# Kernel optimization log

Measured on AMD Instinct MI355X. Metric: run time of the kernel, lower is better.

## Reference

```python
import jax, jax.numpy as jnp
import numpy as np

B, T, D, H = 64, 1024, 1024, 1024  # batch, n_steps, n_in, n_hidden


def setup_inputs() -> dict:
    key = jax.random.key(0)
    k1, k2 = jax.random.split(key)
    x = jax.random.normal(k1, (B, T, D), dtype=jnp.float32)
    # BasicRNNCell kernel: [n_in + n_hidden, n_hidden], glorot-ish scale
    W = jax.random.normal(k2, (D + H, H), dtype=jnp.float32) * (1.0 / np.sqrt(D + H))
    b = jnp.zeros((H,), dtype=jnp.float32)
    return {"x": x, "W": W, "b": b}


def reference(x, W, b):
    """Vanilla RNN (tf BasicRNNCell): h_t = tanh([x_t, h_{t-1}] @ W + b).
    return_last=False -> outputs all hidden states, shape [B, T, H]."""
    Wx = W[: x.shape[-1]]   # [D, H]
    Wh = W[x.shape[-1]:]    # [H, H]
    # Precompute input projections for all steps in one big GEMM: [B, T, H]
    x_proj = jnp.einsum('btd,dh->bth', x, Wx) + b

    def step(h, xp_t):
        h_new = jnp.tanh(xp_t + h @ Wh)
        return h_new, h_new

    h0 = jnp.zeros((x.shape[0], Wh.shape[1]), dtype=x.dtype)
    # scan over time: [T, B, H]
    _, outs = jax.lax.scan(step, h0, jnp.swapaxes(x_proj, 0, 1))
    return jnp.swapaxes(outs, 0, 1)  # [B, T, H]
```

## Files before the change

kernel.cpp:

```cpp
#include <hip/hip_runtime.h>
#include <stdint.h>


#define T_LEN 1024
#define HID   1024

typedef float  f32x4  __attribute__((ext_vector_type(4)));
typedef __bf16 bf16x8 __attribute__((ext_vector_type(8)));
typedef unsigned long long u64;

__global__ __launch_bounds__(256) void xproj_gemm(
    const float* __restrict__ x, const float* __restrict__ W,
    const float* __restrict__ bias, float* __restrict__ out)
{
    __shared__ __align__(16) __bf16 As[128][40];
    __shared__ __align__(16) __bf16 Bs[128][40];

    const int bid = blockIdx.x;
    const int n0  = (bid & 7) << 7;
    const int64_t r0 = (int64_t)(bid >> 3) << 7;
    const int tid  = threadIdx.x;
    const int lane = tid & 63;
    const int w    = tid >> 6;
    const int hi   = lane >> 4, lo = lane & 15;
    const int wm   = (w >> 1) << 6, wn = (w & 1) << 6;

    f32x4 acc[4][4] = {};

    const int arow = tid >> 1, akh = (tid & 1) << 4;
    const int bk   = tid >> 3, bnh = (tid & 7) << 4;

    for (int k0 = 0; k0 < 1024; k0 += 32) {
        {
            const float* src = x + (r0 + arow) * 1024 + k0 + akh;
            bf16x8 t0, t1;
            #pragma unroll
            for (int i2 = 0; i2 < 8; ++i2) { t0[i2] = (__bf16)src[i2]; t1[i2] = (__bf16)src[8 + i2]; }
            *(bf16x8*)&As[arow][akh]     = t0;
            *(bf16x8*)&As[arow][akh + 8] = t1;
        }
        {
            const float* src = W + (int64_t)(k0 + bk) * 1024 + n0 + bnh;
            #pragma unroll
            for (int i2 = 0; i2 < 16; ++i2) {
                int col = bnh + i2;
                Bs[col][bk ^ (((col >> 4) & 3) << 3)] = (__bf16)src[i2];
            }
        }
        __syncthreads();

        bf16x8 af[4], bfr[4];
        #pragma unroll
        for (int f = 0; f < 4; ++f)
            af[f] = *(const bf16x8*)&As[wm + f * 16 + lo][hi << 3];
        #pragma unroll
        for (int f = 0; f < 4; ++f) {
            const int cswz = (((wn >> 4) + f) & 3) << 3;
            bfr[f] = *(const bf16x8*)&Bs[wn + f * 16 + lo][(hi << 3) ^ cswz];
        }
        #pragma unroll
        for (int fm = 0; fm < 4; ++fm)
            #pragma unroll
            for (int fn = 0; fn < 4; ++fn)
                acc[fm][fn] = __builtin_amdgcn_mfma_f32_16x16x32_bf16(af[fm], bfr[fn], acc[fm][fn], 0, 0, 0);
        __syncthreads();
    }

    #pragma unroll
    for (int fm = 0; fm < 4; ++fm) {
        const int64_t mrow = r0 + wm + fm * 16 + hi * 4;
        #pragma unroll
        for (int fn = 0; fn < 4; ++fn) {
            const int col = n0 + wn + fn * 16 + lo;
            const float bv = bias[col];
            #pragma unroll
            for (int r = 0; r < 4; ++r)
                out[(mrow + r) * 1024 + col] = acc[fm][fn][r] + bv;
        }
    }
}

__device__ __forceinline__ float tanh_fast(float x) {
    float e = __builtin_amdgcn_exp2f(x * 2.885390082f);
    return 1.0f - 2.0f * __builtin_amdgcn_rcpf(e + 1.0f);
}

__global__ __launch_bounds__(256) void rnn_scan(
    const float* __restrict__ W, float* __restrict__ out,
    unsigned int* __restrict__ hx)
{
    __shared__ __align__(16) __bf16 WhS[32][64][8];
    __shared__ float red[4][16][17];

    const int bid = blockIdx.x;
    const int ig  = bid >> 6;
    const int jg  = bid & 63;
    const int tid = threadIdx.x;
    const int lane = tid & 63;
    const int w   = tid >> 6;
    const int hi  = lane >> 4, lo = lane & 15;

    for (int kb = w * 8; kb < w * 8 + 8; ++kb) {
        const float* src = W + (int64_t)(1024 + kb * 32 + hi * 8) * 1024 + jg * 16 + lo;
        bf16x8 t;
        #pragma unroll
        for (int ii = 0; ii < 8; ++ii) t[ii] = (__bf16)src[(int64_t)ii * 1024];
        *(bf16x8*)&WhS[kb][lane][0] = t;
    }
    __syncthreads();

    const int64_t rstride = (int64_t)T_LEN * HID;
    const int m = tid >> 4, n = tid & 15;
    float* pobase = out + (int64_t)(ig * 16 + m) * rstride + jg * 16 + n;

    const int rd_row = ig * 16 + lo;
    const int wr_idx = (ig * 16 + m) * 1024 + jg * 16 + n;

    for (int t = 0; t < T_LEN; ++t) {
        float* po = pobase + (int64_t)t * HID;
        float xpv = *po;

        f32x4 acc = {0.f, 0.f, 0.f, 0.f};
        if (t > 0) {
            const unsigned int exptag = (unsigned int)t;
            const u64* bp = (const u64*)(hx + ((t - 1) & 1) * 65536
                                            + rd_row * 1024 + w * 256 + hi * 8);
            u64 q[32];
            bool bad;
            do {
                #pragma unroll
                for (int j = 0; j < 32; ++j)
                    q[j] = __hip_atomic_load(bp + (j >> 2) * 16 + (j & 3),
                                             __ATOMIC_RELAXED, __HIP_MEMORY_SCOPE_AGENT);
                unsigned int badm = 0;
                #pragma unroll
                for (int j = 0; j < 32; ++j) {
                    badm |= ((unsigned int)(q[j] >> 16) & 0xffffu) ^ exptag;
                    badm |= ((unsigned int)(q[j] >> 48)) ^ exptag;
                }
                bad = (badm != 0);
                if (bad) __builtin_amdgcn_s_sleep(1);
            } while (bad);

            #pragma unroll
            for (int kb2 = 0; kb2 < 8; ++kb2) {
                bf16x8 a;
                #pragma unroll
                for (int p = 0; p < 4; ++p) {
                    u64 v = q[kb2 * 4 + p];
                    a[p * 2]     = __builtin_bit_cast(__bf16, (unsigned short)(v & 0xffffu));
                    a[p * 2 + 1] = __builtin_bit_cast(__bf16, (unsigned short)((v >> 32) & 0xffffu));
                }
                acc = __builtin_amdgcn_mfma_f32_16x16x32_bf16(
                          a, *(const bf16x8*)&WhS[w * 8 + kb2][lane][0], acc, 0, 0, 0);
            }
        }

        red[w][hi * 4 + 0][lo] = acc[0];
        red[w][hi * 4 + 1][lo] = acc[1];
        red[w][hi * 4 + 2][lo] = acc[2];
        red[w][hi * 4 + 3][lo] = acc[3];
        __syncthreads();

        float s = red[0][m][n] + red[1][m][n] + red[2][m][n] + red[3][m][n];
        float h = tanh_fast(xpv + s);

        unsigned short hb = __builtin_bit_cast(unsigned short, (__bf16)h);
        __hip_atomic_store(hx + (t & 1) * 65536 + wr_idx,
                           ((unsigned int)(t + 1) << 16) | (unsigned int)hb,
                           __ATOMIC_RELAXED, __HIP_MEMORY_SCOPE_AGENT);

        *po = h;

        __syncthreads();
    }
}

extern "C" void kernel_launch(void* const* d_in, const int* in_sizes, int n_in,
                              void* d_out, int out_size, void* d_ws, size_t ws_size,
                              hipStream_t stream)
{
    const float* x    = (const float*)d_in[0];
    const float* W    = (const float*)d_in[1];
    const float* bias = (const float*)d_in[2];
    float* out = (float*)d_out;

    unsigned int* hx = (unsigned int*)d_ws;

    hipMemsetAsync(hx, 0, 524288, stream);
    xproj_gemm<<<dim3(4096), dim3(256), 0, stream>>>(x, W, bias, out);
    rnn_scan<<<dim3(256), dim3(256), 0, stream>>>(W, out, hx);
}
```

Measured before the change: 8.173 ms.

## Restructure RNN scan into 32 wide blocks with register-resident Wh and LDS-shared h

Replaces the 256-block scan, where each block handled a 16x16 output tile with a cross-wave K split, with 32 blocks of 512 threads. Each wave owns 16 output columns, keeps the full Wh column slice in registers, and runs all of K itself. Each thread loads a small slab of the previous hidden state once, and the slab is shared through swizzled LDS instead of every wave polling 32 words. The goal is fewer blocks spinning on global flags, less redundant L2 polling and no LDS reduction. The cost is far fewer CUs doing the serial per-step work and very high register pressure from holding 32 bf16x8 fragments per thread.

```diff
diff --git a/kernel.cpp b/kernel.cpp
--- a/kernel.cpp
+++ b/kernel.cpp
@@ -85,92 +85,124 @@
     return 1.0f - 2.0f * __builtin_amdgcn_rcpf(e + 1.0f);
 }
 
-__global__ __launch_bounds__(256) void rnn_scan(
+__global__ __launch_bounds__(512, 2) void rnn_scan(
     const float* __restrict__ W, float* __restrict__ out,
     unsigned int* __restrict__ hx)
 {
-    __shared__ __align__(16) __bf16 WhS[32][64][8];
-    __shared__ float red[4][16][17];
+    __shared__ __align__(16) unsigned char A_lds[16 * 2048];
 
     const int bid = blockIdx.x;
-    const int ig  = bid >> 6;
-    const int jg  = bid & 63;
+    const int ig  = bid >> 3;
+    const int jg  = bid & 7;
     const int tid = threadIdx.x;
     const int lane = tid & 63;
-    const int w   = tid >> 6;
+    const int wv  = tid >> 6;
     const int hi  = lane >> 4, lo = lane & 15;
 
-    for (int kb = w * 8; kb < w * 8 + 8; ++kb) {
-        const float* src = W + (int64_t)(1024 + kb * 32 + hi * 8) * 1024 + jg * 16 + lo;
-        bf16x8 t;
-        #pragma unroll
-        for (int ii = 0; ii < 8; ++ii) t[ii] = (__bf16)src[(int64_t)ii * 1024];
-        *(bf16x8*)&WhS[kb][lane][0] = t;
-    }
-    __syncthreads();
+    const int col = jg * 128 + wv * 16 + lo;
+    bf16x8 breg[32];
+    {
+        const float* wb = W + (int64_t)1024 * 1024 + col;
+        #pragma unroll
+        for (int kb = 0; kb < 32; ++kb) {
+            const float* src = wb + (int64_t)(kb * 32 + hi * 8) * 1024;
+            bf16x8 tf;
+            #pragma unroll
+            for (int j = 0; j < 8; ++j) tf[j] = (__bf16)src[(int64_t)j * 1024];
+            breg[kb] = tf;
+        }
+    }
+
+    const int srow = tid >> 5;
+    const int c32  = tid & 31;
+    const int slab_u64 = (ig * 16 + srow) * 512 + c32 * 16;
+    const unsigned swz_w = (unsigned)((srow & 7) << 4);
+    const unsigned kbyte0 = (unsigned)(c32 * 64);
+
+    const unsigned abase = (unsigned)(lo * 2048);
+    const unsigned axor  = (unsigned)((lo & 7) << 4);
 
     const int64_t rstride = (int64_t)T_LEN * HID;
-    const int m = tid >> 4, n = tid & 15;
-    float* pobase = out + (int64_t)(ig * 16 + m) * rstride + jg * 16 + n;
-
-    const int rd_row = ig * 16 + lo;
-    const int wr_idx = (ig * 16 + m) * 1024 + jg * 16 + n;
+    float* pr0 = out + (int64_t)(ig * 16 + hi * 4) * rstride + col;
+    const int wr0 = (ig * 16 + hi * 4) * 1024 + col;
 
     for (int t = 0; t < T_LEN; ++t) {
-        float* po = pobase + (int64_t)t * HID;
-        float xpv = *po;
-
-        f32x4 acc = {0.f, 0.f, 0.f, 0.f};
+        float xpv0 = pr0[(int64_t)t * HID];
+        float xpv1 = pr0[(int64_t)t * HID + rstride];
+        float xpv2 = pr0[(int64_t)t * HID + 2 * rstride];
+        float xpv3 = pr0[(int64_t)t * HID + 3 * rstride];
+
+        f32x4 accs = {0.f, 0.f, 0.f, 0.f};
         if (t > 0) {
             const unsigned int exptag = (unsigned int)t;
-            const u64* bp = (const u64*)(hx + ((t - 1) & 1) * 65536
-                                            + rd_row * 1024 + w * 256 + hi * 8);
-            u64 q[32];
-            bool bad;
-            do {
+            const u64* bp = (const u64*)(hx + ((t - 1) & 1) * 65536) + slab_u64;
+            u64 q[16];
+            #pragma unroll
+            for (int j = 0; j < 16; ++j)
+                q[j] = __hip_atomic_load(bp + j, __ATOMIC_RELAXED, __HIP_MEMORY_SCOPE_AGENT);
+            unsigned bad = 0;
+            #pragma unroll
+            for (int j = 0; j < 16; ++j) {
+                unsigned b = (((unsigned)(q[j] >> 16) & 0xffffu) ^ exptag)
+                           | (((unsigned)(q[j] >> 48)) ^ exptag);
+                bad |= (b ? 1u : 0u) << j;
+            }
+            while (bad) {
+                __builtin_amdgcn_s_sleep(1);
                 #pragma unroll
-                for (int j = 0; j < 32; ++j)
-                    q[j] = __hip_atomic_load(bp + (j >> 2) * 16 + (j & 3),
-                                             __ATOMIC_RELAXED, __HIP_MEMORY_SCOPE_AGENT);
-                unsigned int badm = 0;
-                #pragma unroll
-                for (int j = 0; j < 32; ++j) {
-                    badm |= ((unsigned int)(q[j] >> 16) & 0xffffu) ^ exptag;
-                    badm |= ((unsigned int)(q[j] >> 48)) ^ exptag;
-                }
-                bad = (badm != 0);
-                if (bad) __builtin_amdgcn_s_sleep(1);
-            } while (bad);
-
-            #pragma unroll
-            for (int kb2 = 0; kb2 < 8; ++kb2) {
-                bf16x8 a;
-                #pragma unroll
-                for (int p = 0; p < 4; ++p) {
-                    u64 v = q[kb2 * 4 + p];
-                    a[p * 2]     = __builtin_bit_cast(__bf16, (unsigned short)(v & 0xffffu));
-                    a[p * 2 + 1] = __builtin_bit_cast(__bf16, (unsigned short)((v >> 32) & 0xffffu));
-                }
-                acc = __builtin_amdgcn_mfma_f32_16x16x32_bf16(
-                          a, *(const bf16x8*)&WhS[w * 8 + kb2][lane][0], acc, 0, 0, 0);
-            }
-        }
-
-        red[w][hi * 4 + 0][lo] = acc[0];
-        red[w][hi * 4 + 1][lo] = acc[1];
-        red[w][hi * 4 + 2][lo] = acc[2];
-        red[w][hi * 4 + 3][lo] = acc[3];
-        __syncthreads();
-
-        float s = red[0][m][n] + red[1][m][n] + red[2][m][n] + red[3][m][n];
-        float h = tanh_fast(xpv + s);
-
-        unsigned short hb = __builtin_bit_cast(unsigned short, (__bf16)h);
-        __hip_atomic_store(hx + (t & 1) * 65536 + wr_idx,
-                           ((unsigned int)(t + 1) << 16) | (unsigned int)hb,
-                           __ATOMIC_RELAXED, __HIP_MEMORY_SCOPE_AGENT);
-
-        *po = h;
+                for (int j = 0; j < 16; ++j)
+                    if (bad & (1u << j)) {
+                        q[j] = __hip_atomic_load(bp + j, __ATOMIC_RELAXED, __HIP_MEMORY_SCOPE_AGENT);
+                        if ((((unsigned)(q[j] >> 16) & 0xffffu) == exptag) &&
+                            ((unsigned)(q[j] >> 48) == exptag))
+                            bad &= ~(1u << j);
+                    }
+            }
+            unsigned dw[16];
+            #pragma unroll
+            for (int j = 0; j < 16; ++j)
+                dw[j] = __builtin_amdgcn_perm((unsigned)(q[j] >> 32), (unsigned)q[j], 0x05040100u);
+            #pragma unroll
+            for (int i = 0; i < 4; ++i) {
+                f32x4 v = { __builtin_bit_cast(float, dw[4 * i]),
+                            __builtin_bit_cast(float, dw[4 * i + 1]),
+                            __builtin_bit_cast(float, dw[4 * i + 2]),
+                            __builtin_bit_cast(float, dw[4 * i + 3]) };
+                *(f32x4*)(A_lds + srow * 2048 + ((kbyte0 + 16 * i) ^ swz_w)) = v;
+            }
+            __syncthreads();
+
+            f32x4 acc0 = {0.f, 0.f, 0.f, 0.f}, acc1 = {0.f, 0.f, 0.f, 0.f};
+            #pragma unroll
+            for (int kb = 0; kb < 32; kb += 2) {
+                bf16x8 a0 = *(const bf16x8*)(A_lds + abase + (((unsigned)(kb * 64) + hi * 16) ^ axor));
+                bf16x8 a1 = *(const bf16x8*)(A_lds + abase + (((unsigned)((kb + 1) * 64) + hi * 16) ^ axor));
+                acc0 = __builtin_amdgcn_mfma_f32_16x16x32_bf16(a0, breg[kb],     acc0, 0, 0, 0);
+                acc1 = __builtin_amdgcn_mfma_f32_16x16x32_bf16(a1, breg[kb + 1], acc1, 0, 0, 0);
+            }
+            accs = acc0 + acc1;
+        }
+
+        float h0 = tanh_fast(xpv0 + accs[0]);
+        float h1 = tanh_fast(xpv1 + accs[1]);
+        float h2 = tanh_fast(xpv2 + accs[2]);
+        float h3 = tanh_fast(xpv3 + accs[3]);
+
+        unsigned int* hxs = hx + (t & 1) * 65536 + wr0;
+        const unsigned int tagw = (unsigned int)(t + 1) << 16;
+        __hip_atomic_store(hxs,        tagw | __builtin_bit_cast(unsigned short, (__bf16)h0),
+                           __ATOMIC_RELAXED, __HIP_MEMORY_SCOPE_AGENT);
+        __hip_atomic_store(hxs + 1024, tagw | __builtin_bit_cast(unsigned short, (__bf16)h1),
+                           __ATOMIC_RELAXED, __HIP_MEMORY_SCOPE_AGENT);
+        __hip_atomic_store(hxs + 2048, tagw | __builtin_bit_cast(unsigned short, (__bf16)h2),
+                           __ATOMIC_RELAXED, __HIP_MEMORY_SCOPE_AGENT);
+        __hip_atomic_store(hxs + 3072, tagw | __builtin_bit_cast(unsigned short, (__bf16)h3),
+                           __ATOMIC_RELAXED, __HIP_MEMORY_SCOPE_AGENT);
+
+        pr0[(int64_t)t * HID]               = h0;
+        pr0[(int64_t)t * HID + rstride]     = h1;
+        pr0[(int64_t)t * HID + 2 * rstride] = h2;
+        pr0[(int64_t)t * HID + 3 * rstride] = h3;
 
         __syncthreads();
     }
@@ -189,5 +221,5 @@
 
     hipMemsetAsync(hx, 0, 524288, stream);
     xproj_gemm<<<dim3(4096), dim3(256), 0, stream>>>(x, W, bias, out);
-    rnn_scan<<<dim3(256), dim3(256), 0, stream>>>(W, out, hx);
-}
+    rnn_scan<<<dim3(32), dim3(512), 0, stream>>>(W, out, hx);
+}
```

Result: faster. 8.002 ms (-2.1%).
